# Kernel tuning notes

Hardware: AMD Instinct MI355X
Metric: run time of the kernel (lower is better)

Reference implementation:

```python
import jax, jax.numpy as jnp
import numpy as np

# DCRNN (PEMS-BAY scale) constants
N = 325      # num_nodes
B = 64       # batch_size
T = 12       # encoder seq_len
HZ = 12      # decoder horizon
U = 64       # rnn_units
DIN = 2      # input_dim
DOUT = 1     # output_dim
K = 2        # max_diffusion_step
NM = K + 1   # num diffusion matrices (Chebyshev, single laplacian support)


def _glorot(key, shape):
    lim = float(np.sqrt(6.0 / (shape[0] + shape[1])))
    return jax.random.uniform(key, shape, jnp.float32, -lim, lim)


def setup_inputs() -> dict:
    key = jax.random.key(0)
    ks = jax.random.split(key, 8)
    # random symmetric adjacency -> scaled Laplacian support (lambda_max ~= 2 approx)
    a = np.asarray(jax.random.uniform(ks[0], (N, N)))
    a = (a + a.T) * 0.5
    a = a * (a > 0.9)
    d = a.sum(1)
    dinv = 1.0 / np.sqrt(np.maximum(d, 1e-8))
    L = np.eye(N, dtype=np.float32) - (dinv[:, None] * a * dinv[None, :]).astype(np.float32)
    support = jnp.asarray(L - np.eye(N, dtype=np.float32))  # 2L/lambda_max - I with lambda_max=2

    def cell_params(k, din):
        f = (din + U) * NM
        k1, k2 = jax.random.split(k)
        return dict(gate_W=_glorot(k1, (f, 2 * U)), gate_b=jnp.zeros((2 * U,), jnp.float32),
                    cand_W=_glorot(k2, (f, U)), cand_b=jnp.zeros((U,), jnp.float32))

    inp = {"inputs": jax.random.normal(ks[1], (T, B, N * DIN), jnp.float32),
           "support": support}
    for name, din, kk in [("enc0", DIN, ks[2]), ("enc1", U, ks[3]),
                          ("dec0", DOUT, ks[4]), ("dec1", U, ks[5])]:
        for pn, v in cell_params(kk, din).items():
            inp[f"{name}_{pn}"] = v
    inp["proj_W"] = _glorot(ks[6], (U, DOUT))
    inp["proj_b"] = jnp.zeros((DOUT,), jnp.float32)
    return inp


def _gconv(x, support, W, b):
    # x: (B, N, F). Chebyshev diffusion: x0=x, x1=Lx, x2=2Lx1-x0, ...
    xs = [x]
    x0, x1 = x, jnp.einsum('mn,bnf->bmf', support, x)
    xs.append(x1)
    for _ in range(2, K + 1):
        x2 = 2.0 * jnp.einsum('mn,bnf->bmf', support, x1) - x0
        xs.append(x2)
        x0, x1 = x1, x2
    xk = jnp.concatenate(xs, axis=-1)  # (B, N, NM*F)
    return xk @ W + b


def _gru_cell(x, h, support, gW, gb, cW, cb):
    # diffusion-conv GRU: r,u gates then candidate
    ru = jax.nn.sigmoid(_gconv(jnp.concatenate([x, h], -1), support, gW, gb))
    r, u = jnp.split(ru, 2, axis=-1)
    c = jnp.tanh(_gconv(jnp.concatenate([x, r * h], -1), support, cW, cb))
    return u * h + (1.0 - u) * c


def reference(inputs, support,
              enc0_gate_W, enc0_gate_b, enc0_cand_W, enc0_cand_b,
              enc1_gate_W, enc1_gate_b, enc1_cand_W, enc1_cand_b,
              dec0_gate_W, dec0_gate_b, dec0_cand_W, dec0_cand_b,
              dec1_gate_W, dec1_gate_b, dec1_cand_W, dec1_cand_b,
              proj_W, proj_b):
    x_seq = inputs.reshape(T, B, N, DIN)
    h0 = jnp.zeros((B, N, U), inputs.dtype)

    def enc_step(carry, x):
        h_l0, h_l1 = carry
        h_l0 = _gru_cell(x, h_l0, support, enc0_gate_W, enc0_gate_b, enc0_cand_W, enc0_cand_b)
        h_l1 = _gru_cell(h_l0, h_l1, support, enc1_gate_W, enc1_gate_b, enc1_cand_W, enc1_cand_b)
        return (h_l0, h_l1), None

    (h_l0, h_l1), _ = jax.lax.scan(enc_step, (h0, h0), x_seq)

    def dec_step(carry, _):
        d_in, hd0, hd1 = carry
        hd0 = _gru_cell(d_in, hd0, support, dec0_gate_W, dec0_gate_b, dec0_cand_W, dec0_cand_b)
        hd1 = _gru_cell(hd0, hd1, support, dec1_gate_W, dec1_gate_b, dec1_cand_W, dec1_cand_b)
        out = hd1 @ proj_W + proj_b  # (B, N, DOUT)
        return (out, hd0, hd1), out.reshape(B, N * DOUT)

    start = jnp.zeros((B, N, DOUT), inputs.dtype)  # GO symbol
    _, outputs = jax.lax.scan(dec_step, (start, h_l0, h_l1), None, length=HZ)
    return outputs  # (horizon, B, N*DOUT)
```

## Files before the change

### kernel.cpp

```cpp
#include <hip/hip_runtime.h>

constexpr int N  = 325;
constexpr int B  = 64;
constexpr int T  = 12;
constexpr int HZ = 12;
constexpr int U  = 64;
constexpr int BN = B * N;

constexpr int SSTIL = 42;
constexpr int SSKC  = 11;
constexpr int XST   = 364;

typedef __attribute__((ext_vector_type(8))) short short8;
typedef __attribute__((ext_vector_type(4))) float floatx4;

__device__ inline unsigned short f2bf(float f) {
    unsigned u = __float_as_uint(f);
    u += 0x7fff + ((u >> 16) & 1);
    return (unsigned short)(u >> 16);
}
__device__ inline unsigned pack_hilo(float v) {
    const unsigned short hi = f2bf(v);
    const float hif = __uint_as_float(((unsigned)hi) << 16);
    const unsigned short lo = f2bf(v - hif);
    return (unsigned)hi | ((unsigned)lo << 16);
}
__device__ inline void unpack8(const uint4 u0, const uint4 u1,
                               short8& h, short8& l) {
    const unsigned uu[8] = {u0.x, u0.y, u0.z, u0.w, u1.x, u1.y, u1.z, u1.w};
    #pragma unroll
    for (int j = 0; j < 8; ++j) {
        h[j] = (short)(uu[j] & 0xffffu);
        l[j] = (short)(uu[j] >> 16);
    }
}


__global__ void zero_kernel(unsigned* __restrict__ p, long n) {
    long i = (long)blockIdx.x * blockDim.x + threadIdx.x;
    const long stride = (long)gridDim.x * blockDim.x;
    for (; i < n; i += stride) p[i] = 0u;
}

__global__ __launch_bounds__(256)
void s2_build(const float* __restrict__ S, float* __restrict__ S2)
{
    const int m = blockIdx.x;
    __shared__ float srow[N];
    for (int i = threadIdx.x; i < N; i += 256) srow[i] = S[m * N + i];
    __syncthreads();
    for (int c = threadIdx.x; c < N; c += 256) {
        float a = 0.f;
        for (int k = 0; k < N; ++k) a += srow[k] * S[k * N + c];
        S2[m * N + c] = a;
    }
}

__global__ __launch_bounds__(64)
void prepack_ss(const float* __restrict__ S, const float* __restrict__ S2,
                short* __restrict__ ssh, short* __restrict__ ssl)
{
    const int t = blockIdx.x, kc = blockIdx.y, lane = threadIdx.x;
    const int quad = lane >> 4, l15 = lane & 15;
    short8 hv, lv;
    #pragma unroll
    for (int j = 0; j < 8; ++j) {
        const int m = t * 16 + l15;
        const int k = kc * 32 + quad * 8 + j;
        float v = 0.f;
        if (k < N) {
            if (m < N) v = S[m * N + k];
            else if (m >= 336 && m < 336 + N) v = S2[(m - 336) * N + k];
        }
        const unsigned short hb = f2bf(v);
        hv[j] = (short)hb;
        lv[j] = (short)f2bf(v - __uint_as_float(((unsigned)hb) << 16));
    }
    const size_t off = ((size_t)(t * SSKC + kc) * 64 + lane);
    ((short8*)ssh)[off] = hv;
    ((short8*)ssl)[off] = lv;
}

__global__ __launch_bounds__(64)
void prepack_w(const float* __restrict__ W, short* __restrict__ Wh,
               short* __restrict__ Wl, int F, int Nout, int NT, int Z0KC)
{
    const int kc = blockIdx.x, n = blockIdx.y, lane = threadIdx.x;
    const int quad = lane >> 4, l15 = lane & 15;
    short8 hv, lv;
    #pragma unroll
    for (int j = 0; j < 8; ++j) {
        const int p   = kc * 32 + quad * 8 + j;
        const int col = n * 16 + l15;
        float w = 0.f;
        if (p < Z0KC * 32) {
            const int f = p;
            if (f < F)
                w = W[(size_t)f * Nout + col] - W[(size_t)(2 * F + f) * Nout + col];
        } else {
            const int q = p - Z0KC * 32;
            if (q < F)
                w = W[(size_t)(F + q) * Nout + col];
            else if (q < 2 * F)
                w = 2.f * W[(size_t)(2 * F + (q - F)) * Nout + col];
        }
        const unsigned short hb = f2bf(w);
        hv[j] = (short)hb;
        lv[j] = (short)f2bf(w - __uint_as_float(((unsigned)hb) << 16));
    }
    const size_t off = ((size_t)(kc * NT + n) * 64 + lane);
    ((short8*)Wh)[off] = hv;
    ((short8*)Wl)[off] = lv;
}

template<int DIN, int F, bool RM, bool ZV>
__device__ __forceinline__ void z0_frag(const float* __restrict__ x,
    const float* __restrict__ h, const float* __restrict__ ru,
    int row, int kc, int quad, short8& ah, short8& al)
{
    float v[8];
    if constexpr (ZV) {
        const int k0 = kc * 32 + quad * 8;
        if (k0 < 64) {
            const float4 a = *(const float4*)&x[(size_t)row * 64 + k0];
            const float4 b = *(const float4*)&x[(size_t)row * 64 + k0 + 4];
            v[0]=a.x; v[1]=a.y; v[2]=a.z; v[3]=a.w;
            v[4]=b.x; v[5]=b.y; v[6]=b.z; v[7]=b.w;
        } else {
            const int kk = k0 - 64;
            float4 a = *(const float4*)&h[(size_t)row * 64 + kk];
            float4 b = *(const float4*)&h[(size_t)row * 64 + kk + 4];
            if constexpr (RM) {
                const float4 ra = *(const float4*)&ru[(size_t)row * 128 + kk];
                const float4 rb = *(const float4*)&ru[(size_t)row * 128 + kk + 4];
                a.x *= ra.x; a.y *= ra.y; a.z *= ra.z; a.w *= ra.w;
                b.x *= rb.x; b.y *= rb.y; b.z *= rb.z; b.w *= rb.w;
            }
            v[0]=a.x; v[1]=a.y; v[2]=a.z; v[3]=a.w;
            v[4]=b.x; v[5]=b.y; v[6]=b.z; v[7]=b.w;
        }
    } else {
        #pragma unroll
        for (int j = 0; j < 8; ++j) {
            const int k = kc * 32 + quad * 8 + j;
            float t = 0.f;
            if (k < DIN) t = x[(size_t)row * DIN + k];
            else if (k < F) {
                t = h[(size_t)row * 64 + (k - DIN)];
                if constexpr (RM) t *= ru[(size_t)row * 128 + (k - DIN)];
            }
            v[j] = t;
        }
    }
    #pragma unroll
    for (int j = 0; j < 8; ++j) {
        const unsigned u = pack_hilo(v[j]);
        ah[j] = (short)(u & 0xffffu);
        al[j] = (short)(u >> 16);
    }
}

template<int DIN, int F, int YP, bool RMUL, bool VEC, int NTHR>
__device__ __forceinline__ void diffuse_body(
    const short8* __restrict__ ssh, const short8* __restrict__ ssl,
    const float* __restrict__ x, const float* __restrict__ h,
    const float* __restrict__ ru, unsigned* __restrict__ zcat,
    int c0, int b, int mh, unsigned* __restrict__ xls)
{
    const int tid = threadIdx.x, wave = tid >> 6, lane = tid & 63;
    const int quad = lane >> 4, l15 = lane & 15;

    if constexpr (VEC) {
        for (int idx4 = tid; idx4 < 352 * 8; idx4 += NTHR) {
            const int n = idx4 >> 3, f = (idx4 & 7) * 4, gf = c0 + f;
            uint4 pk = make_uint4(0u, 0u, 0u, 0u);
            if (n < N) {
                const int row = b * N + n;
                float4 v;
                if (gf < DIN) {
                    v = *(const float4*)&x[(size_t)row * DIN + gf];
                } else {
                    v = *(const float4*)&h[(size_t)row * U + (gf - DIN)];
                    if (RMUL) {
                        const float4 rv = *(const float4*)&ru[(size_t)row * 128 + (gf - DIN)];
                        v.x *= rv.x; v.y *= rv.y; v.z *= rv.z; v.w *= rv.w;
                    }
                }
                pk.x = pack_hilo(v.x); pk.y = pack_hilo(v.y);
                pk.z = pack_hilo(v.z); pk.w = pack_hilo(v.w);
            }
            xls[(f + 0) * XST + n] = pk.x;
            xls[(f + 1) * XST + n] = pk.y;
            xls[(f + 2) * XST + n] = pk.z;
            xls[(f + 3) * XST + n] = pk.w;
        }
    } else {
        for (int idx = tid; idx < 352 * 32; idx += NTHR) {
            const int n = idx >> 5, f = idx & 31, gf = c0 + f;
            unsigned u = 0u;
            if (n < N && gf < F) {
                const int row = b * N + n;
                float v;
                if (gf < DIN) {
                    v = x[(size_t)row * DIN + gf];
                } else {
                    v = h[(size_t)row * U + (gf - DIN)];
                    if (RMUL) v *= ru[(size_t)row * 128 + (gf - DIN)];
                }
                u = pack_hilo(v);
            }
            xls[f * XST + n] = u;
        }
    }
    __syncthreads();

    const int tb = mh * 21 + wave * 3;

    floatx4 acc[3][2];
    #pragma unroll
    for (int i = 0; i < 3; ++i)
        #pragma unroll
        for (int n = 0; n < 2; ++n)
            acc[i][n] = (floatx4){0.f, 0.f, 0.f, 0.f};

    short8 cah[3], cal[3], nah[3], nal[3];
    #pragma unroll
    for (int i = 0; i < 3; ++i) {
        const size_t fo = (size_t)((tb + i) * SSKC) * 64 + lane;
        cah[i] = ssh[fo]; cal[i] = ssl[fo];
    }
    for (int kc = 0; kc < SSKC; ++kc) {
        if (kc + 1 < SSKC) {
            #pragma unroll
            for (int i = 0; i < 3; ++i) {
                const size_t fo = (size_t)((tb + i) * SSKC + kc + 1) * 64 + lane;
                nah[i] = ssh[fo]; nal[i] = ssl[fo];
            }
        }
        short8 bh[2], bl[2];
        const int koff = kc * 32 + quad * 8;
        #pragma unroll
        for (int n = 0; n < 2; ++n) {
            const uint4 u0 = *(const uint4*)&xls[(n * 16 + l15) * XST + koff];
            const uint4 u1 = *(const uint4*)&xls[(n * 16 + l15) * XST + koff + 4];
            unpack8(u0, u1, bh[n], bl[n]);
        }
        #pragma unroll
        for (int i = 0; i < 3; ++i)
            #pragma unroll
            for (int n = 0; n < 2; ++n) {
                acc[i][n] = __builtin_amdgcn_mfma_f32_16x16x32_bf16(cah[i], bh[n], acc[i][n], 0, 0, 0);
                acc[i][n] = __builtin_amdgcn_mfma_f32_16x16x32_bf16(cah[i], bl[n], acc[i][n], 0, 0, 0);
                acc[i][n] = __builtin_amdgcn_mfma_f32_16x16x32_bf16(cal[i], bh[n], acc[i][n], 0, 0, 0);
            }
        if (kc + 1 < SSKC) {
            #pragma unroll
            for (int i = 0; i < 3; ++i) { cah[i] = nah[i]; cal[i] = nal[i]; }
        }
    }

    #pragma unroll
    for (int i = 0; i < 3; ++i) {
        const int t = tb + i;
        #pragma unroll
        for (int n = 0; n < 2; ++n) {
            const int col = c0 + n * 16 + l15;
            if (col >= F) continue;
            #pragma unroll
            for (int r = 0; r < 4; ++r) {
                const int m = t * 16 + quad * 4 + r;
                if (m < N)
                    zcat[(size_t)(b * N + m) * YP + col] = pack_hilo(acc[i][n][r]);
                else if (m >= 336 && m < 336 + N)
                    zcat[(size_t)(b * N + (m - 336)) * YP + F + col] = pack_hilo(acc[i][n][r]);
            }
        }
    }
}


template<int DIN, int F, int Z0KC, int YKC, bool ZV>
__device__ __forceinline__ void gate_body(const unsigned* __restrict__ zcat,
    const float* __restrict__ x, const float* __restrict__ h,
    const short8* __restrict__ Wh, const short8* __restrict__ Wl,
    const float* __restrict__ bias, float* __restrict__ ruout, int bx, int nb)
{
    constexpr int YP = YKC * 32, NT = 4;
    const int tid = threadIdx.x, wave = tid >> 6, lane = tid & 63;
    const int quad = lane >> 4, l15 = lane & 15;
    const int row0 = bx * 64 + wave * 16;
    const int row = row0 + l15;

    floatx4 acc[NT];
    #pragma unroll
    for (int n = 0; n < NT; ++n) {
        const float bv = bias[(nb + n) * 16 + l15];
        acc[n] = (floatx4){bv, bv, bv, bv};
    }
    for (int kc = 0; kc < Z0KC; ++kc) {
        short8 ahi, alo;
        z0_frag<DIN, F, false, ZV>(x, h, nullptr, row, kc, quad, ahi, alo);
        const short8* __restrict__ wh = Wh + (size_t)(kc * 8 + nb) * 64 + lane;
        const short8* __restrict__ wl = Wl + (size_t)(kc * 8 + nb) * 64 + lane;
        #pragma unroll
        for (int n = 0; n < NT; ++n) {
            const short8 bh = wh[n * 64], bl = wl[n * 64];
            acc[n] = __builtin_amdgcn_mfma_f32_16x16x32_bf16(ahi, bh, acc[n], 0, 0, 0);
            acc[n] = __builtin_amdgcn_mfma_f32_16x16x32_bf16(ahi, bl, acc[n], 0, 0, 0);
            acc[n] = __builtin_amdgcn_mfma_f32_16x16x32_bf16(alo, bh, acc[n], 0, 0, 0);
        }
    }
    const unsigned* __restrict__ zrow = zcat + (size_t)row * YP + quad * 8;
    for (int kc = 0; kc < YKC; ++kc) {
        const uint4* p = (const uint4*)(zrow + kc * 32);
        short8 ahi, alo;
        unpack8(p[0], p[1], ahi, alo);
        const short8* __restrict__ wh = Wh + (size_t)((Z0KC + kc) * 8 + nb) * 64 + lane;
        const short8* __restrict__ wl = Wl + (size_t)((Z0KC + kc) * 8 + nb) * 64 + lane;
        #pragma unroll
        for (int n = 0; n < NT; ++n) {
            const short8 bh = wh[n * 64], bl = wl[n * 64];
            acc[n] = __builtin_amdgcn_mfma_f32_16x16x32_bf16(ahi, bh, acc[n], 0, 0, 0);
            acc[n] = __builtin_amdgcn_mfma_f32_16x16x32_bf16(ahi, bl, acc[n], 0, 0, 0);
            acc[n] = __builtin_amdgcn_mfma_f32_16x16x32_bf16(alo, bh, acc[n], 0, 0, 0);
        }
    }
    #pragma unroll
    for (int n = 0; n < NT; ++n) {
        const int col = (nb + n) * 16 + l15;
        #pragma unroll
        for (int r = 0; r < 4; ++r) {
            const int rw = row0 + quad * 4 + r;
            ruout[(size_t)rw * 128 + col] = 1.f / (1.f + __expf(-acc[n][r]));
        }
    }
}

template<int DIN, int F, int Z0KC, int YKC, bool ZV>
__device__ __forceinline__ void cand_body(const unsigned* __restrict__ zcat,
    const float* __restrict__ x, const float* __restrict__ h,
    const float* __restrict__ ru, const short8* __restrict__ Wh,
    const short8* __restrict__ Wl, const float* __restrict__ bias,
    float* __restrict__ hout, int bx, int nb)
{
    constexpr int YP = YKC * 32, NT = 2;
    const int tid = threadIdx.x, wave = tid >> 6, lane = tid & 63;
    const int quad = lane >> 4, l15 = lane & 15;
    const int row0 = bx * 64 + wave * 16;
    const int row = row0 + l15;

    floatx4 acc[NT];
    #pragma unroll
    for (int n = 0; n < NT; ++n) {
        const float bv = bias[(nb + n) * 16 + l15];
        acc[n] = (floatx4){bv, bv, bv, bv};
    }
    for (int kc = 0; kc < Z0KC; ++kc) {
        short8 ahi, alo;
        z0_frag<DIN, F, true, ZV>(x, h, ru, row, kc, quad, ahi, alo);
        const short8* __restrict__ wh = Wh + (size_t)(kc * 4 + nb) * 64 + lane;
        const short8* __restrict__ wl = Wl + (size_t)(kc * 4 + nb) * 64 + lane;
        #pragma unroll
        for (int n = 0; n < NT; ++n) {
            const short8 bh = wh[n * 64], bl = wl[n * 64];
            acc[n] = __builtin_amdgcn_mfma_f32_16x16x32_bf16(ahi, bh, acc[n], 0, 0, 0);
            acc[n] = __builtin_amdgcn_mfma_f32_16x16x32_bf16(ahi, bl, acc[n], 0, 0, 0);
            acc[n] = __builtin_amdgcn_mfma_f32_16x16x32_bf16(alo, bh, acc[n], 0, 0, 0);
        }
    }
    const unsigned* __restrict__ zrow = zcat + (size_t)row * YP + quad * 8;
    for (int kc = 0; kc < YKC; ++kc) {
        const uint4* p = (const uint4*)(zrow + kc * 32);
        short8 ahi, alo;
        unpack8(p[0], p[1], ahi, alo);
        const short8* __restrict__ wh = Wh + (size_t)((Z0KC + kc) * 4 + nb) * 64 + lane;
        const short8* __restrict__ wl = Wl + (size_t)((Z0KC + kc) * 4 + nb) * 64 + lane;
        #pragma unroll
        for (int n = 0; n < NT; ++n) {
            const short8 bh = wh[n * 64], bl = wl[n * 64];
            acc[n] = __builtin_amdgcn_mfma_f32_16x16x32_bf16(ahi, bh, acc[n], 0, 0, 0);
            acc[n] = __builtin_amdgcn_mfma_f32_16x16x32_bf16(ahi, bl, acc[n], 0, 0, 0);
            acc[n] = __builtin_amdgcn_mfma_f32_16x16x32_bf16(alo, bh, acc[n], 0, 0, 0);
        }
    }
    #pragma unroll
    for (int n = 0; n < NT; ++n) {
        const int col = (nb + n) * 16 + l15;
        #pragma unroll
        for (int r = 0; r < 4; ++r) {
            const int rw = row0 + quad * 4 + r;
            const float c  = tanhf(acc[n][r]);
            const float ug = ru[(size_t)rw * 128 + 64 + col];
            const float hv = h[(size_t)rw * 64 + col];
            hout[(size_t)rw * 64 + col] = ug * hv + (1.f - ug) * c;
        }
    }
}


template<int DIN, int F, int YP, bool RMUL, int C0OFF, bool VEC>
__global__ __launch_bounds__(448, 3)
void diffuse_solo(const short8* __restrict__ ssh, const short8* __restrict__ ssl,
                  const float* __restrict__ x, const float* __restrict__ h,
                  const float* __restrict__ ru, unsigned* __restrict__ zcat)
{
    __shared__ __align__(16) unsigned xls[32 * XST];
    diffuse_body<DIN, F, YP, RMUL, VEC, 448>(ssh, ssl, x, h, ru, zcat,
                                             C0OFF + blockIdx.x * 32, blockIdx.y,
                                             blockIdx.z, xls);
}

template<int DIN, int F, int Z0KC, int YKC, bool ZV>
__global__ __launch_bounds__(256)
void gate_cell(const unsigned* __restrict__ zcat, const float* __restrict__ x,
               const float* __restrict__ h, const short8* __restrict__ Wh,
               const short8* __restrict__ Wl, const float* __restrict__ bias,
               float* __restrict__ ru)
{
    gate_body<DIN, F, Z0KC, YKC, ZV>(zcat, x, h, Wh, Wl, bias, ru,
                                     blockIdx.x, blockIdx.y * 4);
}

template<int DIN, int F, int Z0KC, int YKC, bool ZV>
__global__ __launch_bounds__(256)
void cand_cell(const unsigned* __restrict__ zcat, const float* __restrict__ x,
               const float* __restrict__ h, const float* __restrict__ ru,
               const short8* __restrict__ Wh, const short8* __restrict__ Wl,
               const float* __restrict__ bias, float* __restrict__ hout)
{
    cand_body<DIN, F, Z0KC, YKC, ZV>(zcat, x, h, ru, Wh, Wl, bias, hout,
                                     blockIdx.x, blockIdx.y * 2);
}

__global__ __launch_bounds__(256)
void cand_proj(const unsigned* __restrict__ zcat, const float* __restrict__ x,
               const float* __restrict__ h, const float* __restrict__ ru,
               const short8* __restrict__ Wh, const short8* __restrict__ Wl,
               const float* __restrict__ bias, float* __restrict__ hout,
               const float* __restrict__ pW, const float* __restrict__ pb,
               float* __restrict__ outp, float* __restrict__ dec_in)
{
    constexpr int Z0KC = 4, YKC = 8, YP = 256, NT = 4;
    const int tid = threadIdx.x, wave = tid >> 6, lane = tid & 63;
    const int quad = lane >> 4, l15 = lane & 15;
    const int row0 = blockIdx.x * 64 + wave * 16;
    const int row = row0 + l15;

    floatx4 acc[NT];
    #pragma unroll
    for (int n = 0; n < NT; ++n) {
        const float bv = bias[n * 16 + l15];
        acc[n] = (floatx4){bv, bv, bv, bv};
    }
    for (int kc = 0; kc < Z0KC; ++kc) {
        short8 ahi, alo;
        z0_frag<64, 128, true, true>(x, h, ru, row, kc, quad, ahi, alo);
        const short8* __restrict__ wh = Wh + (size_t)(kc * 4) * 64 + lane;
        const short8* __restrict__ wl = Wl + (size_t)(kc * 4) * 64 + lane;
        #pragma unroll
        for (int n = 0; n < NT; ++n) {
            const short8 bh = wh[n * 64], bl = wl[n * 64];
            acc[n] = __builtin_amdgcn_mfma_f32_16x16x32_bf16(ahi, bh, acc[n], 0, 0, 0);
            acc[n] = __builtin_amdgcn_mfma_f32_16x16x32_bf16(ahi, bl, acc[n], 0, 0, 0);
            acc[n] = __builtin_amdgcn_mfma_f32_16x16x32_bf16(alo, bh, acc[n], 0, 0, 0);
        }
    }
    const unsigned* __restrict__ zrow = zcat + (size_t)row * YP + quad * 8;
    for (int kc = 0; kc < YKC; ++kc) {
        const uint4* p = (const uint4*)(zrow + kc * 32);
        short8 ahi, alo;
        unpack8(p[0], p[1], ahi, alo);
        const short8* __restrict__ wh = Wh + (size_t)((Z0KC + kc) * 4) * 64 + lane;
        const short8* __restrict__ wl = Wl + (size_t)((Z0KC + kc) * 4) * 64 + lane;
        #pragma unroll
        for (int n = 0; n < NT; ++n) {
            const short8 bh = wh[n * 64], bl = wl[n * 64];
            acc[n] = __builtin_amdgcn_mfma_f32_16x16x32_bf16(ahi, bh, acc[n], 0, 0, 0);
            acc[n] = __builtin_amdgcn_mfma_f32_16x16x32_bf16(ahi, bl, acc[n], 0, 0, 0);
            acc[n] = __builtin_amdgcn_mfma_f32_16x16x32_bf16(alo, bh, acc[n], 0, 0, 0);
        }
    }
    float pr[4] = {0.f, 0.f, 0.f, 0.f};
    #pragma unroll
    for (int n = 0; n < NT; ++n) {
        const int col = n * 16 + l15;
        const float pw = pW[col];
        #pragma unroll
        for (int r = 0; r < 4; ++r) {
            const int rw = row0 + quad * 4 + r;
            const float c  = tanhf(acc[n][r]);
            const float ug = ru[(size_t)rw * 128 + 64 + col];
            const float hv = h[(size_t)rw * 64 + col];
            const float hn = ug * hv + (1.f - ug) * c;
            hout[(size_t)rw * 64 + col] = hn;
            pr[r] += hn * pw;
        }
    }
    #pragma unroll
    for (int r = 0; r < 4; ++r) {
        float v = pr[r];
        v += __shfl_xor(v, 1); v += __shfl_xor(v, 2);
        v += __shfl_xor(v, 4); v += __shfl_xor(v, 8);
        if (l15 == 0) {
            const int rw = row0 + quad * 4 + r;
            const float o = v + pb[0];
            outp[rw]   = o;
            dec_in[rw] = o;
        }
    }
}


struct DuoDP {
    const short8 *ssh, *ssl;
    const float *xA, *hA, *ruA; unsigned* zA;
    const float *xB, *hB, *ruB; unsigned* zB;
    int cA;
    int coA;
    int coB;
};

__global__ __launch_bounds__(896, 7)
void diffuse_duo_g(DuoDP P)
{
    __shared__ __align__(16) unsigned xls[32 * XST];
    if ((int)blockIdx.x < P.cA)
        diffuse_body<2, 66, 160, false, false, 896>(P.ssh, P.ssl, P.xA, P.hA,
                                                    nullptr, P.zA,
                                                    P.coA + blockIdx.x * 32,
                                                    blockIdx.y, 0, xls);
    else
        diffuse_body<64, 128, 256, false, true, 896>(P.ssh, P.ssl, P.xB, P.hB,
                                                     nullptr, P.zB,
                                                     P.coB + (blockIdx.x - P.cA) * 32,
                                                     blockIdx.y, 0, xls);
}

__global__ __launch_bounds__(448, 3)
void diffuse_duo_c(DuoDP P)
{
    __shared__ __align__(16) unsigned xls[32 * XST];
    if ((int)blockIdx.x < P.cA)
        diffuse_body<2, 66, 160, true, false, 448>(P.ssh, P.ssl, P.xA, P.hA,
                                                   P.ruA, P.zA,
                                                   P.coA + blockIdx.x * 32,
                                                   blockIdx.y, blockIdx.z, xls);
    else
        diffuse_body<64, 128, 256, true, true, 448>(P.ssh, P.ssl, P.xB, P.hB,
                                                    P.ruB, P.zB,
                                                    P.coB + (blockIdx.x - P.cA) * 32,
                                                    blockIdx.y, blockIdx.z, xls);
}

__global__ __launch_bounds__(448, 3)
void diffuse_duo_dec(DuoDP P)
{
    __shared__ __align__(16) unsigned xls[32 * XST];
    if ((int)blockIdx.x < P.cA)
        diffuse_body<1, 65, 160, false, false, 448>(P.ssh, P.ssl, P.xA, P.hA,
                                                    nullptr, P.zA,
                                                    P.coA + blockIdx.x * 32,
                                                    blockIdx.y, blockIdx.z, xls);
    else
        diffuse_body<64, 128, 256, false, true, 448>(P.ssh, P.ssl, P.xB, P.hB,
                                                     nullptr, P.zB,
                                                     P.coB + (blockIdx.x - P.cA) * 32,
                                                     blockIdx.y, blockIdx.z, xls);
}

struct DuoGP {
    const unsigned* zA; const float *xA, *hA;
    const short8 *WhA, *WlA; const float* bA; float* ruA;
    const unsigned* zB; const float *xB, *hB;
    const short8 *WhB, *WlB; const float* bB; float* ruB;
};

__global__ __launch_bounds__(256)
void gate_duo(DuoGP P)
{
    if (blockIdx.z == 0)
        gate_body<2, 66, 3, 5, false>(P.zA, P.xA, P.hA, P.WhA, P.WlA, P.bA,
                                      P.ruA, blockIdx.x, blockIdx.y * 4);
    else
        gate_body<64, 128, 4, 8, true>(P.zB, P.xB, P.hB, P.WhB, P.WlB, P.bB,
                                       P.ruB, blockIdx.x, blockIdx.y * 4);
}

struct DuoCP {
    const unsigned* zA; const float *xA, *hA, *ruA;
    const short8 *WhA, *WlA; const float* bA; float* hoA;
    const unsigned* zB; const float *xB, *hB, *ruB;
    const short8 *WhB, *WlB; const float* bB; float* hoB;
};

__global__ __launch_bounds__(256)
void cand_duo(DuoCP P)
{
    if (blockIdx.z == 0)
        cand_body<2, 66, 3, 5, false>(P.zA, P.xA, P.hA, P.ruA, P.WhA, P.WlA,
                                      P.bA, P.hoA, blockIdx.x, blockIdx.y * 2);
    else
        cand_body<64, 128, 4, 8, true>(P.zB, P.xB, P.hB, P.ruB, P.WhB, P.WlB,
                                       P.bB, P.hoB, blockIdx.x, blockIdx.y * 2);
}


extern "C" void kernel_launch(void* const* d_in, const int* in_sizes, int n_in,
                              void* d_out, int out_size, void* d_ws, size_t ws_size,
                              hipStream_t stream)
{
    const float* inputs = (const float*)d_in[0];
    const float* S      = (const float*)d_in[1];
    const float* Wt[4][4];
    for (int l = 0; l < 4; ++l)
        for (int j = 0; j < 4; ++j)
            Wt[l][j] = (const float*)d_in[2 + l * 4 + j];
    const float* pW = (const float*)d_in[18];
    const float* pb = (const float*)d_in[19];
    float* out = (float*)d_out;

    float*    ws     = (float*)d_ws;
    float*    H0[2]  = {ws, ws + (size_t)BN * U};
    float*    H1[2]  = {ws + 2 * (size_t)BN * U, ws + 3 * (size_t)BN * U};
    float*    dec_in = ws + 4 * (size_t)BN * U;
    float*    ruA    = dec_in + BN;
    float*    ruB    = ruA + (size_t)BN * 128;
    unsigned* zcatA  = (unsigned*)(ruB + (size_t)BN * 128);
    unsigned* zcatB  = zcatA + (size_t)BN * 160;
    float*    S2     = (float*)(zcatB + (size_t)BN * 256);
    char*     pp     = (char*)(S2 + (size_t)N * N);
    pp = (char*)(((uintptr_t)pp + 15) & ~(uintptr_t)15);

    short* ssh = (short*)pp;
    short* ssl = ssh + (size_t)SSTIL * SSKC * 64 * 8;
    char*  wpbase = (char*)(ssl + (size_t)SSTIL * SSKC * 64 * 8);

    const int Fs[4]   = {66, 128, 65, 128};
    const int KPs[4]  = {256, 384, 256, 384};
    const int Z0s[4]  = {3, 4, 3, 4};
    short *Wgh[4], *Wgl[4], *Wch[4], *Wcl[4];
    size_t off = 0;
    for (int l = 0; l < 4; ++l) {
        const size_t ge = (size_t)KPs[l] * 128, ce = (size_t)KPs[l] * 64;
        Wgh[l] = (short*)(wpbase + off); off += ge * 2;
        Wgl[l] = (short*)(wpbase + off); off += ge * 2;
        Wch[l] = (short*)(wpbase + off); off += ce * 2;
        Wcl[l] = (short*)(wpbase + off); off += ce * 2;
    }

    const long zn = (long)BN * (4 * U) + BN + (long)BN * 256 + (long)BN * (160 + 256);
    zero_kernel<<<2048, 256, 0, stream>>>((unsigned*)ws, zn);

    s2_build<<<N, 256, 0, stream>>>(S, S2);
    prepack_ss<<<dim3(SSTIL, SSKC), 64, 0, stream>>>(S, S2, ssh, ssl);
    for (int l = 0; l < 4; ++l) {
        prepack_w<<<dim3(KPs[l] / 32, 8), 64, 0, stream>>>(Wt[l][0], Wgh[l], Wgl[l],
                                                           Fs[l], 128, 8, Z0s[l]);
        prepack_w<<<dim3(KPs[l] / 32, 4), 64, 0, stream>>>(Wt[l][2], Wch[l], Wcl[l],
                                                           Fs[l], 64, 4, Z0s[l]);
    }

    const short8* SSH = (const short8*)ssh;
    const short8* SSL = (const short8*)ssl;
    int p0 = 0, p1 = 0;

    for (int s = 0; s <= T; ++s) {
        const float* x0 = inputs + (size_t)s * BN * 2;
        const bool a = (s < T), b1 = (s >= 1);
        if (a && b1) {
            DuoDP dp{SSH, SSL, x0, H0[p0], nullptr, zcatA,
                     H0[p0], H1[p1], nullptr, zcatB, 3, 0, 0};
            diffuse_duo_g<<<dim3(7, B), 896, 0, stream>>>(dp);
            DuoGP gp{zcatA, x0, H0[p0], (short8*)Wgh[0], (short8*)Wgl[0], Wt[0][1], ruA,
                     zcatB, H0[p0], H1[p1], (short8*)Wgh[1], (short8*)Wgl[1], Wt[1][1], ruB};
            gate_duo<<<dim3(BN / 64, 2, 2), 256, 0, stream>>>(gp);
            DuoDP dp2{SSH, SSL, x0, H0[p0], ruA, zcatA,
                      H0[p0], H1[p1], ruB, zcatB, 2, 2, 64};
            diffuse_duo_c<<<dim3(4, B, 2), 448, 0, stream>>>(dp2);
            DuoCP cp{zcatA, x0, H0[p0], ruA, (short8*)Wch[0], (short8*)Wcl[0], Wt[0][3], H0[p0 ^ 1],
                     zcatB, H0[p0], H1[p1], ruB, (short8*)Wch[1], (short8*)Wcl[1], Wt[1][3], H1[p1 ^ 1]};
            cand_duo<<<dim3(BN / 64, 2, 2), 256, 0, stream>>>(cp);
            p0 ^= 1; p1 ^= 1;
        } else if (a) {
            diffuse_solo<2, 66, 160, false, 0, false><<<dim3(3, B, 2), 448, 0, stream>>>(
                SSH, SSL, x0, H0[p0], nullptr, zcatA);
            gate_cell<2, 66, 3, 5, false><<<dim3(BN / 64, 2), 256, 0, stream>>>(
                zcatA, x0, H0[p0], (short8*)Wgh[0], (short8*)Wgl[0], Wt[0][1], ruA);
            diffuse_solo<2, 66, 160, true, 2, false><<<dim3(2, B, 2), 448, 0, stream>>>(
                SSH, SSL, x0, H0[p0], ruA, zcatA);
            cand_cell<2, 66, 3, 5, false><<<dim3(BN / 64, 2), 256, 0, stream>>>(
                zcatA, x0, H0[p0], ruA, (short8*)Wch[0], (short8*)Wcl[0], Wt[0][3], H0[p0 ^ 1]);
            p0 ^= 1;
        } else {
            diffuse_solo<64, 128, 256, false, 0, true><<<dim3(4, B, 2), 448, 0, stream>>>(
                SSH, SSL, H0[p0], H1[p1], nullptr, zcatB);
            gate_cell<64, 128, 4, 8, true><<<dim3(BN / 64, 2), 256, 0, stream>>>(
                zcatB, H0[p0], H1[p1], (short8*)Wgh[1], (short8*)Wgl[1], Wt[1][1], ruB);
            diffuse_solo<64, 128, 256, true, 64, true><<<dim3(2, B, 2), 448, 0, stream>>>(
                SSH, SSL, H0[p0], H1[p1], ruB, zcatB);
            cand_cell<64, 128, 4, 8, true><<<dim3(BN / 64, 2), 256, 0, stream>>>(
                zcatB, H0[p0], H1[p1], ruB, (short8*)Wch[1], (short8*)Wcl[1], Wt[1][3], H1[p1 ^ 1]);
            p1 ^= 1;
        }
    }

    for (int hz = 0; hz < HZ; ++hz) {
        DuoDP dd{SSH, SSL, dec_in, H0[p0], nullptr, zcatA,
                 H0[p0], H1[p1], nullptr, zcatB, 3, 0, 64};
        diffuse_duo_dec<<<dim3(5, B, 2), 448, 0, stream>>>(dd);
        gate_cell<1, 65, 3, 5, false><<<dim3(BN / 64, 2), 256, 0, stream>>>(
            zcatA, dec_in, H0[p0], (short8*)Wgh[2], (short8*)Wgl[2], Wt[2][1], ruA);
        diffuse_solo<1, 65, 160, true, 1, false><<<dim3(2, B, 2), 448, 0, stream>>>(
            SSH, SSL, dec_in, H0[p0], ruA, zcatA);
        cand_cell<1, 65, 3, 5, false><<<dim3(BN / 64, 2), 256, 0, stream>>>(
            zcatA, dec_in, H0[p0], ruA, (short8*)Wch[2], (short8*)Wcl[2], Wt[2][3], H0[p0 ^ 1]);
        p0 ^= 1;
        diffuse_solo<64, 128, 256, false, 0, true><<<dim3(2, B, 2), 448, 0, stream>>>(
            SSH, SSL, H0[p0], H1[p1], nullptr, zcatB);
        gate_cell<64, 128, 4, 8, true><<<dim3(BN / 64, 2), 256, 0, stream>>>(
            zcatB, H0[p0], H1[p1], (short8*)Wgh[3], (short8*)Wgl[3], Wt[3][1], ruA);
        diffuse_solo<64, 128, 256, true, 64, true><<<dim3(2, B, 2), 448, 0, stream>>>(
            SSH, SSL, H0[p0], H1[p1], ruA, zcatB);
        cand_proj<<<BN / 64, 256, 0, stream>>>(
            zcatB, H0[p0], H1[p1], ruA, (short8*)Wch[3], (short8*)Wcl[3], Wt[3][3],
            H1[p1 ^ 1], pW, pb, out + (size_t)hz * BN, dec_in);
        p1 ^= 1;
    }
}
```

Before: 3.721 ms.

## Share h0 diffusion between stacked layers and skip zero-state diffusion at step zero

In the paired encoder step, the layer-0 diffusion blocks now also write their diffused h0 columns into layer 1's concatenation buffer. Layer 1 therefore only diffuses its own hidden-state columns, which drops the grid from 7 to 5 column blocks. At the first encoder step the hidden state is known to be zero, so the gate diffusion launches only the column block holding the input features and the candidate diffusion launch is removed. The step-zero shortcut relies on the h columns of zcatA already holding zeros (or values equivalent to diffusing zero), which depends on how that buffer was initialised.

```diff
diff --git a/kernel.cpp b/kernel.cpp
--- a/kernel.cpp
+++ b/kernel.cpp
@@ -160,12 +160,13 @@
     }
 }
 
-template<int DIN, int F, int YP, bool RMUL, bool VEC, int NTHR>
+template<int DIN, int F, int YP, bool RMUL, bool VEC, int NTHR, bool DUAL = false>
 __device__ __forceinline__ void diffuse_body(
     const short8* __restrict__ ssh, const short8* __restrict__ ssl,
     const float* __restrict__ x, const float* __restrict__ h,
     const float* __restrict__ ru, unsigned* __restrict__ zcat,
-    int c0, int b, int mh, unsigned* __restrict__ xls)
+    int c0, int b, int mh, unsigned* __restrict__ xls,
+    unsigned* __restrict__ zdual = nullptr)
 {
     const int tid = threadIdx.x, wave = tid >> 6, lane = tid & 63;
     const int quad = lane >> 4, l15 = lane & 15;
@@ -269,10 +270,22 @@
             #pragma unroll
             for (int r = 0; r < 4; ++r) {
                 const int m = t * 16 + quad * 4 + r;
-                if (m < N)
-                    zcat[(size_t)(b * N + m) * YP + col] = pack_hilo(acc[i][n][r]);
-                else if (m >= 336 && m < 336 + N)
-                    zcat[(size_t)(b * N + (m - 336)) * YP + F + col] = pack_hilo(acc[i][n][r]);
+                const unsigned pv = pack_hilo(acc[i][n][r]);
+                if (m < N) {
+                    zcat[(size_t)(b * N + m) * YP + col] = pv;
+                    if constexpr (DUAL) {
+                        const int j = col - DIN;
+                        if (j >= 0)
+                            zdual[(size_t)(b * N + m) * 256 + j] = pv;
+                    }
+                } else if (m >= 336 && m < 336 + N) {
+                    zcat[(size_t)(b * N + (m - 336)) * YP + F + col] = pv;
+                    if constexpr (DUAL) {
+                        const int j = col - DIN;
+                        if (j >= 0)
+                            zdual[(size_t)(b * N + (m - 336)) * 256 + 128 + j] = pv;
+                    }
+                }
             }
         }
     }
@@ -524,16 +537,14 @@
 void diffuse_duo_g(DuoDP P)
 {
     __shared__ __align__(16) unsigned xls[32 * XST];
-    if ((int)blockIdx.x < P.cA)
-        diffuse_body<2, 66, 160, false, false, 896>(P.ssh, P.ssl, P.xA, P.hA,
-                                                    nullptr, P.zA,
-                                                    P.coA + blockIdx.x * 32,
-                                                    blockIdx.y, 0, xls);
+    if ((int)blockIdx.x < 3)
+        diffuse_body<2, 66, 160, false, false, 896, true>(
+            P.ssh, P.ssl, P.xA, P.hA, nullptr, P.zA,
+            blockIdx.x * 32, blockIdx.y, 0, xls, P.zB);
     else
-        diffuse_body<64, 128, 256, false, true, 896>(P.ssh, P.ssl, P.xB, P.hB,
-                                                     nullptr, P.zB,
-                                                     P.coB + (blockIdx.x - P.cA) * 32,
-                                                     blockIdx.y, 0, xls);
+        diffuse_body<64, 128, 256, false, true, 896>(
+            P.ssh, P.ssl, P.xB, P.hB, nullptr, P.zB,
+            64 + (blockIdx.x - 3) * 32, blockIdx.y, 0, xls);
 }
 
 __global__ __launch_bounds__(448, 3)
@@ -670,7 +681,7 @@
         if (a && b1) {
             DuoDP dp{SSH, SSL, x0, H0[p0], nullptr, zcatA,
                      H0[p0], H1[p1], nullptr, zcatB, 3, 0, 0};
-            diffuse_duo_g<<<dim3(7, B), 896, 0, stream>>>(dp);
+            diffuse_duo_g<<<dim3(5, B), 896, 0, stream>>>(dp);
             DuoGP gp{zcatA, x0, H0[p0], (short8*)Wgh[0], (short8*)Wgl[0], Wt[0][1], ruA,
                      zcatB, H0[p0], H1[p1], (short8*)Wgh[1], (short8*)Wgl[1], Wt[1][1], ruB};
             gate_duo<<<dim3(BN / 64, 2, 2), 256, 0, stream>>>(gp);
@@ -682,12 +693,10 @@
             cand_duo<<<dim3(BN / 64, 2, 2), 256, 0, stream>>>(cp);
             p0 ^= 1; p1 ^= 1;
         } else if (a) {
-            diffuse_solo<2, 66, 160, false, 0, false><<<dim3(3, B, 2), 448, 0, stream>>>(
+            diffuse_solo<2, 66, 160, false, 0, false><<<dim3(1, B, 2), 448, 0, stream>>>(
                 SSH, SSL, x0, H0[p0], nullptr, zcatA);
             gate_cell<2, 66, 3, 5, false><<<dim3(BN / 64, 2), 256, 0, stream>>>(
                 zcatA, x0, H0[p0], (short8*)Wgh[0], (short8*)Wgl[0], Wt[0][1], ruA);
-            diffuse_solo<2, 66, 160, true, 2, false><<<dim3(2, B, 2), 448, 0, stream>>>(
-                SSH, SSL, x0, H0[p0], ruA, zcatA);
             cand_cell<2, 66, 3, 5, false><<<dim3(BN / 64, 2), 256, 0, stream>>>(
                 zcatA, x0, H0[p0], ruA, (short8*)Wch[0], (short8*)Wcl[0], Wt[0][3], H0[p0 ^ 1]);
             p0 ^= 1;
```

After: 4.083 ms. 1.1x slower.
